# Performance work log

Hardware: AMD Instinct MI355X
Metric: run time of the kernel (lower is better)

## Reference

```python
import math
import jax, jax.numpy as jnp
import numpy as np

EMBED_DIM = 512
NUM_CLASSES = 100000
BATCH = 1024
SCALE = 64.0
MARGIN = 0.5
EASY_MARGIN = False

COS_M = math.cos(MARGIN)
SIN_M = math.sin(MARGIN)
TH = math.cos(math.pi - MARGIN)
MM = math.sin(math.pi - MARGIN) * MARGIN


def setup_inputs() -> dict:
    key = jax.random.key(0)
    k1, k2, k3 = jax.random.split(key, 3)
    embeddings = jax.random.normal(k1, (BATCH, EMBED_DIM), dtype=jnp.float32)
    labels = jax.random.randint(k2, (BATCH,), 0, NUM_CLASSES, dtype=jnp.int64)
    # xavier_uniform over (num_classes, embedding_dim)
    limit = math.sqrt(6.0 / (NUM_CLASSES + EMBED_DIM))
    weight = jax.random.uniform(k3, (NUM_CLASSES, EMBED_DIM), dtype=jnp.float32,
                                minval=-limit, maxval=limit)
    return {"embeddings": embeddings, "labels": labels, "weight": weight}


def _l2norm(x, eps=1e-12):
    # matches torch F.normalize(p=2): x / max(||x||, eps)
    n = jnp.sqrt(jnp.sum(x * x, axis=1, keepdims=True))
    return x / jnp.maximum(n, eps)


def reference(embeddings, labels, weight):
    emb = _l2norm(embeddings)            # (B, D)
    w = _l2norm(weight)                  # (C, D)
    cos_theta = emb @ w.T                # (B, C)
    cos_theta = jnp.clip(cos_theta, -1.0 + 1e-07, 1.0 - 1e-07)
    sin_theta = jnp.sqrt(1.0 - cos_theta * cos_theta)
    cos_theta_m = cos_theta * COS_M - sin_theta * SIN_M
    if EASY_MARGIN:
        cos_theta_m = jnp.where(cos_theta > 0, cos_theta_m, cos_theta)
    else:
        cos_theta_m = jnp.where(cos_theta > TH, cos_theta_m, cos_theta - MM)
    # one-hot blend: margin applied only at target column per row
    one_hot = (jnp.arange(NUM_CLASSES)[None, :] == labels[:, None])  # (B, C) bool
    logits = jnp.where(one_hot, cos_theta_m, cos_theta) * SCALE
    return logits
```

## Files before the change

### kernel.cpp

```cpp
#include <hip/hip_runtime.h>
#include <hip/hip_bf16.h>

#define NCLS   100000
#define NPAD   100096
#define BATCH  1024
#define EDIM   512

#define COS_M_  0.8775825618903728f
#define SIN_M_  0.479425538604203f
#define TH_     (-0.8775825618903728f)
#define MM_     0.2397127693021015f
#define SCALE_  64.0f

typedef __attribute__((ext_vector_type(8))) short short8;
typedef __attribute__((ext_vector_type(4))) float f32x4;

__device__ __forceinline__ ushort f2bf(float f) {
    uint u = __float_as_uint(f);
    u += 0x7fffu + ((u >> 16) & 1u);
    return (ushort)(u >> 16);
}

__global__ __launch_bounds__(256) void norm_all_kernel(
    const float* __restrict__ emb, const float* __restrict__ wgt,
    ushort* __restrict__ Ebf, ushort* __restrict__ Wbf)
{
    int gw   = (int)((blockIdx.x * blockDim.x + threadIdx.x) >> 6);
    int lane = (int)(threadIdx.x & 63);
    const float* ip;
    ushort* op;
    if (gw < BATCH) {
        ip = emb + (size_t)gw * EDIM + lane * 8;
        op = Ebf + (size_t)gw * EDIM + lane * 8;
    } else {
        int wr = gw - BATCH;
        if (wr >= NPAD) return;
        op = Wbf + (size_t)wr * EDIM + lane * 8;
        if (wr >= NCLS) {
            uint4 z = make_uint4(0u, 0u, 0u, 0u);
            *(uint4*)op = z;
            return;
        }
        ip = wgt + (size_t)wr * EDIM + lane * 8;
    }
    float4 x0 = *(const float4*)ip;
    float4 x1 = *(const float4*)(ip + 4);
    float ss = x0.x*x0.x + x0.y*x0.y + x0.z*x0.z + x0.w*x0.w
             + x1.x*x1.x + x1.y*x1.y + x1.z*x1.z + x1.w*x1.w;
    #pragma unroll
    for (int off = 32; off; off >>= 1) ss += __shfl_xor(ss, off, 64);
    float inv = 1.0f / fmaxf(sqrtf(ss), 1e-12f);
    uint w0 = (uint)f2bf(x0.x*inv) | ((uint)f2bf(x0.y*inv) << 16);
    uint w1 = (uint)f2bf(x0.z*inv) | ((uint)f2bf(x0.w*inv) << 16);
    uint w2 = (uint)f2bf(x1.x*inv) | ((uint)f2bf(x1.y*inv) << 16);
    uint w3 = (uint)f2bf(x1.z*inv) | ((uint)f2bf(x1.w*inv) << 16);
    uint4 r; r.x = w0; r.y = w1; r.z = w2; r.w = w3;
    *(uint4*)op = r;
}

__global__ __launch_bounds__(256) void fixup_labels_kernel(
    const int* __restrict__ labels, float* __restrict__ C)
{
    int row = (int)(blockIdx.x * blockDim.x + threadIdx.x);
    if (row >= BATCH) return;
    int lab = labels[row];
    float* p = C + (size_t)row * NCLS + lab;
    float c = *p * (1.0f / SCALE_);
    float s  = sqrtf(1.0f - c * c);
    float cm = c * COS_M_ - s * SIN_M_;
    cm = (c > TH_) ? cm : (c - MM_);
    *p = cm * SCALE_;
}

#define GLL16(g, s) __builtin_amdgcn_global_load_lds(                    \
    (const __attribute__((address_space(1))) void*)(g),                  \
    (__attribute__((address_space(3))) void*)(s), 16, 0, 0)

__global__ __launch_bounds__(256, 4) void gemm_arc_kernel(
    const ushort* __restrict__ A,
    const ushort* __restrict__ B,
    float* __restrict__ C)
{
    __shared__ __align__(16) ushort Als[2][128 * 32];
    __shared__ __align__(16) ushort Bls[2][128 * 32];

    const int t    = (int)threadIdx.x;
    const int lane = t & 63;
    const int w    = t >> 6;
    const int wrow = w >> 1, wcol = w & 1;
    const int lr   = lane & 15, lg = lane >> 4;

    const int nwg  = (int)gridDim.x;
    const int cpx  = nwg >> 3;
    const int bid  = (int)blockIdx.x;
    const int swz  = (bid & 7) * cpx + (bid >> 3);
    const int brow = swz & 7;
    const int bcol = swz >> 3;

    const f32x4 z4 = {0.f, 0.f, 0.f, 0.f};
    f32x4 acc[4][4];
    #pragma unroll
    for (int i = 0; i < 4; ++i)
        #pragma unroll
        for (int j = 0; j < 4; ++j) acc[i][j] = z4;

    const int srow = t >> 2;
    const int scb  = ((t & 3) * 16) ^ (((t >> 3) & 3) << 4);
    const char* Ab = (const char*)(A + ((size_t)brow * 128 + srow) * EDIM) + scb;
    const char* Bb = (const char*)(B + ((size_t)bcol * 128 + srow) * EDIM) + scb;
    const uint ldsw = (uint)w * 1024;

    const int kswz  = ((lr >> 1) & 3) << 4;
    const int aoff0 = (wrow * 64 + lr) * 64 + ((lg * 16) ^ kswz);
    const int boff0 = (wcol * 64 + lr) * 64 + ((lg * 16) ^ kswz);

#define STAGE(c, kt) do {                                                  \
        const char* a0 = Ab + (kt) * 64;                                   \
        const char* b0 = Bb + (kt) * 64;                                   \
        char* Ad = (char*)Als + (size_t)(c) * 8192 + ldsw;                 \
        char* Bd = (char*)Bls + (size_t)(c) * 8192 + ldsw;                 \
        GLL16(a0,                 Ad);                                     \
        GLL16(a0 + 64 * EDIM * 2, Ad + 4096);                              \
        GLL16(b0,                 Bd);                                     \
        GLL16(b0 + 64 * EDIM * 2, Bd + 4096);                              \
    } while (0)

#define COMPUTE(c) do {                                                    \
        const char* Ap = (const char*)Als + (size_t)(c) * 8192;            \
        const char* Bp = (const char*)Bls + (size_t)(c) * 8192;            \
        short8 av[4], bv[4];                                               \
        _Pragma("unroll")                                                  \
        for (int mi = 0; mi < 4; ++mi)                                     \
            av[mi] = *(const short8*)(Ap + aoff0 + mi * 1024);             \
        _Pragma("unroll")                                                  \
        for (int ni = 0; ni < 4; ++ni)                                     \
            bv[ni] = *(const short8*)(Bp + boff0 + ni * 1024);             \
        _Pragma("unroll")                                                  \
        for (int mi = 0; mi < 4; ++mi)                                     \
            _Pragma("unroll")                                              \
            for (int ni = 0; ni < 4; ++ni)                                 \
                acc[mi][ni] = __builtin_amdgcn_mfma_f32_16x16x32_bf16(     \
                    bv[ni], av[mi], acc[mi][ni], 0, 0, 0);                 \
    } while (0)

    STAGE(0, 0);

    #pragma unroll
    for (int kt = 0; kt < 15; ++kt) {
        asm volatile("s_waitcnt lgkmcnt(0)" ::: "memory");
        __builtin_amdgcn_s_barrier();
        STAGE((kt + 1) & 1, kt + 1);
        asm volatile("s_waitcnt vmcnt(4)" ::: "memory");
        __builtin_amdgcn_s_barrier();
        COMPUTE(kt & 1);
    }
    asm volatile("s_waitcnt vmcnt(0)" ::: "memory");
    __builtin_amdgcn_s_barrier();
    COMPUTE(15 & 1);

    const int mbase = brow * 128 + wrow * 64;
    const int nbase = bcol * 128 + wcol * 64;
    #pragma unroll
    for (int mi = 0; mi < 4; ++mi) {
        const int grow = mbase + mi * 16 + lr;
        float* crow = C + (size_t)grow * NCLS;
        #pragma unroll
        for (int ni = 0; ni < 4; ++ni) {
            if (nbase + ni * 16 < NCLS) {
                f32x4 v = acc[mi][ni];
                f32x4 o;
                #pragma unroll
                for (int j = 0; j < 4; ++j) {
                    float cc = fminf(fmaxf(v[j], -1.0f + 1e-7f), 1.0f - 1e-7f);
                    o[j] = cc * SCALE_;
                }
                __builtin_nontemporal_store(o,
                    (f32x4*)&crow[nbase + ni * 16 + lg * 4]);
            }
        }
    }
#undef STAGE
#undef COMPUTE
}

extern "C" void kernel_launch(void* const* d_in, const int* in_sizes, int n_in,
                              void* d_out, int out_size, void* d_ws, size_t ws_size,
                              hipStream_t stream)
{
    const float* emb    = (const float*)d_in[0];
    const int*   labels = (const int*)d_in[1];
    const float* wgt    = (const float*)d_in[2];
    float*       out    = (float*)d_out;

    ushort* Ebf = (ushort*)d_ws;
    ushort* Wbf = (ushort*)((char*)d_ws + (size_t)BATCH * EDIM * 2);

    norm_all_kernel<<<(BATCH + NPAD) / 4, 256, 0, stream>>>(emb, wgt, Ebf, Wbf);

    gemm_arc_kernel<<<(BATCH / 128) * (NPAD / 128), 256, 0, stream>>>(Ebf, Wbf, out);

    fixup_labels_kernel<<<BATCH / 256, 256, 0, stream>>>(labels, out);
}
```

Baseline: 221.6 us.

## Fuse label margin into GEMM epilogue and triple-buffer B tiles

The GEMM epilogue now applies the ArcFace margin to each row's target column, so the separate fixup kernel launch and its read-modify-write of the output go away. The B operand moves from double to triple buffering in LDS and is prefetched two k-steps ahead, with vmcnt waits adjusted to match. This aims to hide more global-load latency and remove one launch. In exchange it uses more LDS per block, which may lower occupancy, and adds a label load plus a branch in the epilogue.

```diff
diff --git a/kernel.cpp b/kernel.cpp
--- a/kernel.cpp
+++ b/kernel.cpp
@@ -58,20 +58,6 @@
     *(uint4*)op = r;
 }
 
-__global__ __launch_bounds__(256) void fixup_labels_kernel(
-    const int* __restrict__ labels, float* __restrict__ C)
-{
-    int row = (int)(blockIdx.x * blockDim.x + threadIdx.x);
-    if (row >= BATCH) return;
-    int lab = labels[row];
-    float* p = C + (size_t)row * NCLS + lab;
-    float c = *p * (1.0f / SCALE_);
-    float s  = sqrtf(1.0f - c * c);
-    float cm = c * COS_M_ - s * SIN_M_;
-    cm = (c > TH_) ? cm : (c - MM_);
-    *p = cm * SCALE_;
-}
-
 #define GLL16(g, s) __builtin_amdgcn_global_load_lds(                    \
     (const __attribute__((address_space(1))) void*)(g),                  \
     (__attribute__((address_space(3))) void*)(s), 16, 0, 0)
@@ -79,10 +65,11 @@
 __global__ __launch_bounds__(256, 4) void gemm_arc_kernel(
     const ushort* __restrict__ A,
     const ushort* __restrict__ B,
+    const int* __restrict__ labels,
     float* __restrict__ C)
 {
     __shared__ __align__(16) ushort Als[2][128 * 32];
-    __shared__ __align__(16) ushort Bls[2][128 * 32];
+    __shared__ __align__(16) ushort Bls[3][128 * 32];
 
     const int t    = (int)threadIdx.x;
     const int lane = t & 63;
@@ -114,20 +101,22 @@
     const int aoff0 = (wrow * 64 + lr) * 64 + ((lg * 16) ^ kswz);
     const int boff0 = (wcol * 64 + lr) * 64 + ((lg * 16) ^ kswz);
 
-#define STAGE(c, kt) do {                                                  \
+#define STAGE_A(c, kt) do {                                                \
         const char* a0 = Ab + (kt) * 64;                                   \
-        const char* b0 = Bb + (kt) * 64;                                   \
         char* Ad = (char*)Als + (size_t)(c) * 8192 + ldsw;                 \
-        char* Bd = (char*)Bls + (size_t)(c) * 8192 + ldsw;                 \
         GLL16(a0,                 Ad);                                     \
         GLL16(a0 + 64 * EDIM * 2, Ad + 4096);                              \
+    } while (0)
+#define STAGE_B(c, kt) do {                                                \
+        const char* b0 = Bb + (kt) * 64;                                   \
+        char* Bd = (char*)Bls + (size_t)(c) * 8192 + ldsw;                 \
         GLL16(b0,                 Bd);                                     \
         GLL16(b0 + 64 * EDIM * 2, Bd + 4096);                              \
     } while (0)
 
-#define COMPUTE(c) do {                                                    \
-        const char* Ap = (const char*)Als + (size_t)(c) * 8192;            \
-        const char* Bp = (const char*)Bls + (size_t)(c) * 8192;            \
+#define COMPUTE(ca, cb) do {                                               \
+        const char* Ap = (const char*)Als + (size_t)(ca) * 8192;           \
+        const char* Bp = (const char*)Bls + (size_t)(cb) * 8192;           \
         short8 av[4], bv[4];                                               \
         _Pragma("unroll")                                                  \
         for (int mi = 0; mi < 4; ++mi)                                     \
@@ -143,30 +132,38 @@
                     bv[ni], av[mi], acc[mi][ni], 0, 0, 0);                 \
     } while (0)
 
-    STAGE(0, 0);
-
-    #pragma unroll
-    for (int kt = 0; kt < 15; ++kt) {
+    STAGE_B(0, 0);
+    STAGE_A(0, 0);
+    STAGE_B(1, 1);
+
+    #pragma unroll
+    for (int kt = 0; kt < 16; ++kt) {
         asm volatile("s_waitcnt lgkmcnt(0)" ::: "memory");
         __builtin_amdgcn_s_barrier();
-        STAGE((kt + 1) & 1, kt + 1);
-        asm volatile("s_waitcnt vmcnt(4)" ::: "memory");
+        if (kt < 15) STAGE_A((kt + 1) & 1, kt + 1);
+        if (kt < 14) STAGE_B((kt + 2) % 3, kt + 2);
+        if (kt <= 13) {
+            asm volatile("s_waitcnt vmcnt(6)" ::: "memory");
+        } else if (kt == 14) {
+            asm volatile("s_waitcnt vmcnt(4)" ::: "memory");
+        } else {
+            asm volatile("s_waitcnt vmcnt(0)" ::: "memory");
+        }
         __builtin_amdgcn_s_barrier();
-        COMPUTE(kt & 1);
+        COMPUTE(kt & 1, kt % 3);
     }
-    asm volatile("s_waitcnt vmcnt(0)" ::: "memory");
-    __builtin_amdgcn_s_barrier();
-    COMPUTE(15 & 1);
 
     const int mbase = brow * 128 + wrow * 64;
     const int nbase = bcol * 128 + wcol * 64;
     #pragma unroll
     for (int mi = 0; mi < 4; ++mi) {
         const int grow = mbase + mi * 16 + lr;
+        const int lab  = labels[grow];
         float* crow = C + (size_t)grow * NCLS;
         #pragma unroll
         for (int ni = 0; ni < 4; ++ni) {
             if (nbase + ni * 16 < NCLS) {
+                const int c0 = nbase + ni * 16 + lg * 4;
                 f32x4 v = acc[mi][ni];
                 f32x4 o;
                 #pragma unroll
@@ -174,12 +171,25 @@
                     float cc = fminf(fmaxf(v[j], -1.0f + 1e-7f), 1.0f - 1e-7f);
                     o[j] = cc * SCALE_;
                 }
-                __builtin_nontemporal_store(o,
-                    (f32x4*)&crow[nbase + ni * 16 + lg * 4]);
+                const int d = lab - c0;
+                if ((unsigned)d < 4u) {
+                    float cv = (d == 0) ? v[0] : (d == 1) ? v[1]
+                             : (d == 2) ? v[2] : v[3];
+                    float cc = fminf(fmaxf(cv, -1.0f + 1e-7f), 1.0f - 1e-7f);
+                    float s  = sqrtf(1.0f - cc * cc);
+                    float cm = cc * COS_M_ - s * SIN_M_;
+                    cm = (cc > TH_) ? cm : (cc - MM_);
+                    cm *= SCALE_;
+                    #pragma unroll
+                    for (int j = 0; j < 4; ++j)
+                        o[j] = (d == j) ? cm : o[j];
+                }
+                __builtin_nontemporal_store(o, (f32x4*)&crow[c0]);
             }
         }
     }
-#undef STAGE
+#undef STAGE_A
+#undef STAGE_B
 #undef COMPUTE
 }
 
@@ -197,7 +207,5 @@
 
     norm_all_kernel<<<(BATCH + NPAD) / 4, 256, 0, stream>>>(emb, wgt, Ebf, Wbf);
 
-    gemm_arc_kernel<<<(BATCH / 128) * (NPAD / 128), 256, 0, stream>>>(Ebf, Wbf, out);
-
-    fixup_labels_kernel<<<BATCH / 256, 256, 0, stream>>>(labels, out);
-}
+    gemm_arc_kernel<<<(BATCH / 128) * (NPAD / 128), 256, 0, stream>>>(Ebf, Wbf, labels, out);
+}
```

Result: no change. 223.7 us (+0.9%).
